# Performance work log

Hardware: AMD Instinct MI355X
Metric: run time of the kernel (lower is better)

## Reference

```python
import jax, jax.numpy as jnp
import numpy as np
from math import sqrt


def setup_inputs() -> dict:
    key = jax.random.key(0)
    k1, k2, k3, k4, k5 = jax.random.split(key, 5)
    B, L, H, D = 16, 4096, 16, 64
    S, M = 4096, 256
    queries = jax.random.normal(k1, (B, L, H, D), dtype=jnp.float32)
    keys = jax.random.normal(k2, (B, S, H, D), dtype=jnp.float32)
    values = jax.random.normal(k3, (B, S, H, D), dtype=jnp.float32)
    # nn.Linear(L_k=S, M): weight [M, S], bias [M]
    squeeze_w = jax.random.normal(k4, (M, S), dtype=jnp.float32) / sqrt(S)
    squeeze_b = jax.random.normal(k5, (M,), dtype=jnp.float32) * 0.01
    return {"queries": queries, "keys": keys, "values": values,
            "squeeze_w": squeeze_w, "squeeze_b": squeeze_b}


def reference(queries, keys, values, squeeze_w, squeeze_b):
    # queries: [B,L,H,D]; keys/values: [B,S,H,D]; squeeze_w: [M,S]; squeeze_b: [M]
    B, L, H, D = queries.shape
    scale = 1.0 / sqrt(D)
    bias = squeeze_b[None, :, None, None]  # broadcast over [B,M,H,D]
    # Linear over the sequence axis S -> M (Linformer compression)
    keys_sq = jnp.einsum('bshd,ms->bmhd', keys, squeeze_w) + bias      # [B,M,H,D]
    values_sq = jnp.einsum('bshd,ms->bmhd', values, squeeze_w) + bias  # [B,M,H,D]
    # Scaled dot-product attention against compressed K/V
    attn = jnp.einsum('blhd,bmhd->bhlm', queries, keys_sq) * scale     # [B,H,L,M]
    attn = jax.nn.softmax(attn, axis=-1)  # dropout is identity in eval / p=0
    context = jnp.einsum('bhlm,bmhd->blhd', attn, values_sq)           # [B,L,H,D]
    return context
```

## Files before the change

kernel.cpp:

```cpp
#include <hip/hip_runtime.h>

#define NB 16
#define NL 4096
#define NH 16
#define ND 64
#define NS 4096
#define NM 256

typedef __fp16 f16;
typedef __attribute__((ext_vector_type(8)))  __fp16 f16x8;
typedef __attribute__((ext_vector_type(4)))  __fp16 f16x4;
typedef __attribute__((ext_vector_type(2)))  __fp16 f16x2;
typedef __attribute__((ext_vector_type(4)))  float  f32x4;
typedef __attribute__((ext_vector_type(16))) float  f32x16;

__device__ __forceinline__ void gload_lds16(const void* g, void* l) {
  __builtin_amdgcn_global_load_lds(
      (const __attribute__((address_space(1))) void*)g,
      (__attribute__((address_space(3))) void*)l, 16, 0, 0);
}

__device__ __forceinline__ int pk2(float a, float b) {
  f16x2 t = __builtin_amdgcn_cvt_pkrtz(a, b);
  union { f16x2 h; int i; } u; u.h = t; return u.i;
}

__global__ __launch_bounds__(256) void k_wcvt(const float* __restrict__ W,
                                              f16* __restrict__ Wk) {
  const int o  = blockIdx.x * 256 + threadIdx.x;
  const int m  = o & 255;
  const int kb = o >> 8;
  const float* src = W + (long)m * NS + kb * 8;
  f32x4 v0 = *(const f32x4*)(src);
  f32x4 v1 = *(const f32x4*)(src + 4);
  union { f16x8 v; f16x2 h2[4]; } pk;
  pk.h2[0] = __builtin_amdgcn_cvt_pkrtz(v0[0], v0[1]);
  pk.h2[1] = __builtin_amdgcn_cvt_pkrtz(v0[2], v0[3]);
  pk.h2[2] = __builtin_amdgcn_cvt_pkrtz(v1[0], v1[1]);
  pk.h2[3] = __builtin_amdgcn_cvt_pkrtz(v1[2], v1[3]);
  *(f16x8*)(Wk + (long)o * 8) = pk.v;
}

__global__ __launch_bounds__(512, 4) void k_squeeze(
    const f16* __restrict__ Wk, const float* __restrict__ keys,
    const float* __restrict__ values, const float* __restrict__ bias,
    f16* __restrict__ Ksq, f16* __restrict__ Vsq) {
  const int h = blockIdx.x & 15;
  const int b = (blockIdx.x >> 4) & 15;
  const int t = blockIdx.x >> 8;
  const float* __restrict__ X = t ? values : keys;

  __shared__ __align__(16) f16 XT0[64 * 72];
  __shared__ __align__(16) f16 XT1[64 * 72];

  const int tid  = threadIdx.x;
  const int lane = tid & 63;
  const int w    = tid >> 6;
  const int l31  = lane & 31;
  const int g    = lane >> 5;

  const int sp = tid & 31;
  const int ng = tid >> 5;
  const float* Xb = X + ((long)b * NS) * (NH * ND) + h * ND;

  f32x16 acc[2];
#pragma unroll
  for (int di = 0; di < 2; ++di)
#pragma unroll
    for (int r = 0; r < 16; ++r) acc[di][r] = 0.f;

  f32x4 xrA[2], xrB[2];
#pragma unroll
  for (int r = 0; r < 2; ++r)
    xrA[r] = *(const f32x4*)(Xb + (long)(2 * sp + r) * (NH * ND) + ng * 4);
#pragma unroll
  for (int r = 0; r < 2; ++r)
    xrB[r] = *(const f32x4*)(Xb + (long)(64 + 2 * sp + r) * (NH * ND) + ng * 4);

  const f16* Wlane = Wk + ((long)g * 256 + w * 32 + l31) * 8;

  for (int kt2 = 0; kt2 < 32; ++kt2) {
    {
      const int kt = 2 * kt2;
      f16x8 af[4];
#pragma unroll
      for (int ks = 0; ks < 4; ++ks)
        af[ks] = *(const f16x8*)(Wlane + ((long)(kt * 8 + ks * 2) * 256) * 8);
      int p0 = pk2(xrA[0][0], xrA[1][0]);
      int p1 = pk2(xrA[0][1], xrA[1][1]);
      int p2 = pk2(xrA[0][2], xrA[1][2]);
      int p3 = pk2(xrA[0][3], xrA[1][3]);
      if (kt2 < 31) {
#pragma unroll
        for (int r = 0; r < 2; ++r)
          xrA[r] = *(const f32x4*)(Xb + (long)((kt + 2) * 64 + 2 * sp + r) * (NH * ND) + ng * 4);
      }
      *(int*)((char*)XT0 + (ng * 4 + 0) * 144 + sp * 4) = p0;
      *(int*)((char*)XT0 + (ng * 4 + 1) * 144 + sp * 4) = p1;
      *(int*)((char*)XT0 + (ng * 4 + 2) * 144 + sp * 4) = p2;
      *(int*)((char*)XT0 + (ng * 4 + 3) * 144 + sp * 4) = p3;
      __syncthreads();
#pragma unroll
      for (int ks = 0; ks < 4; ++ks) {
        f16x8 bf0 = *(const f16x8*)((const char*)XT0 + l31 * 144 + ks * 32 + g * 16);
        f16x8 bf1 = *(const f16x8*)((const char*)XT0 + (32 + l31) * 144 + ks * 32 + g * 16);
        acc[0] = __builtin_amdgcn_mfma_f32_32x32x16_f16(af[ks], bf0, acc[0], 0, 0, 0);
        acc[1] = __builtin_amdgcn_mfma_f32_32x32x16_f16(af[ks], bf1, acc[1], 0, 0, 0);
      }
    }
    {
      const int kt = 2 * kt2 + 1;
      f16x8 af[4];
#pragma unroll
      for (int ks = 0; ks < 4; ++ks)
        af[ks] = *(const f16x8*)(Wlane + ((long)(kt * 8 + ks * 2) * 256) * 8);
      int p0 = pk2(xrB[0][0], xrB[1][0]);
      int p1 = pk2(xrB[0][1], xrB[1][1]);
      int p2 = pk2(xrB[0][2], xrB[1][2]);
      int p3 = pk2(xrB[0][3], xrB[1][3]);
      if (kt2 < 31) {
#pragma unroll
        for (int r = 0; r < 2; ++r)
          xrB[r] = *(const f32x4*)(Xb + (long)((kt + 2) * 64 + 2 * sp + r) * (NH * ND) + ng * 4);
      }
      *(int*)((char*)XT1 + (ng * 4 + 0) * 144 + sp * 4) = p0;
      *(int*)((char*)XT1 + (ng * 4 + 1) * 144 + sp * 4) = p1;
      *(int*)((char*)XT1 + (ng * 4 + 2) * 144 + sp * 4) = p2;
      *(int*)((char*)XT1 + (ng * 4 + 3) * 144 + sp * 4) = p3;
      __syncthreads();
#pragma unroll
      for (int ks = 0; ks < 4; ++ks) {
        f16x8 bf0 = *(const f16x8*)((const char*)XT1 + l31 * 144 + ks * 32 + g * 16);
        f16x8 bf1 = *(const f16x8*)((const char*)XT1 + (32 + l31) * 144 + ks * 32 + g * 16);
        acc[0] = __builtin_amdgcn_mfma_f32_32x32x16_f16(af[ks], bf0, acc[0], 0, 0, 0);
        acc[1] = __builtin_amdgcn_mfma_f32_32x32x16_f16(af[ks], bf1, acc[1], 0, 0, 0);
      }
    }
  }

  const long bh = b * 16 + h;
  if (t == 0) {
    f16* K = Ksq + bh * (NM * ND);
#pragma unroll
    for (int di = 0; di < 2; ++di)
#pragma unroll
      for (int r = 0; r < 16; ++r) {
        const int m = w * 32 + (r & 3) + 8 * (r >> 2) + 4 * g;
        const int d = di * 32 + l31;
        K[((d >> 3) * 256 + m) * 8 + (d & 7)] = (f16)(acc[di][r] + bias[m]);
      }
  } else {
    f16* V = Vsq + bh * (ND * NM);
#pragma unroll
    for (int di = 0; di < 2; ++di)
#pragma unroll
      for (int qq = 0; qq < 4; ++qq) {
        const int m0 = w * 32 + 8 * qq + 4 * g;
        const int d  = di * 32 + l31;
        f16x2 p0 = __builtin_amdgcn_cvt_pkrtz(acc[di][qq * 4 + 0] + bias[m0 + 0],
                                              acc[di][qq * 4 + 1] + bias[m0 + 1]);
        f16x2 p1 = __builtin_amdgcn_cvt_pkrtz(acc[di][qq * 4 + 2] + bias[m0 + 2],
                                              acc[di][qq * 4 + 3] + bias[m0 + 3]);
        f16x4 pv; pv[0] = p0[0]; pv[1] = p0[1]; pv[2] = p1[0]; pv[3] = p1[1];
        *(f16x4*)(V + ((m0 >> 3) * 64 + d) * 8 + 4 * g) = pv;
      }
  }
}

__global__ __launch_bounds__(256, 2) void k_attn(const float* __restrict__ Q,
                                                 const f16* __restrict__ Ksq,
                                                 const f16* __restrict__ Vsq,
                                                 float* __restrict__ Out) {
  const int xcd   = blockIdx.x & 7;
  const int local = blockIdx.x >> 3;
  const int bh    = xcd * 32 + (local >> 1);
  const int chunk = local & 1;
  const int b = bh >> 4, h = bh & 15;

  __shared__ __align__(16) f16 Klds[8 * 256 * 8];
  __shared__ __align__(16) f16 Vlds[32 * 64 * 8];

  const int tid = threadIdx.x, lane = tid & 63, w = tid >> 6;
  const int q = lane & 31, hi = lane >> 5;

  const float* Qlane = Q   + (((long)b * NL + q) * NH + h) * ND;
  float*       Olane = Out + (((long)b * NL + q) * NH + h) * ND;
  const float  c = 0.125f * 1.44269504088896f;

  f32x4 qv[8];
  {
    const float* qp = Qlane + (long)(chunk * 2048 + w * 32) * (NH * ND) + hi * 8;
#pragma unroll
    for (int kt = 0; kt < 4; ++kt) {
      qv[2 * kt]     = *(const f32x4*)(qp + kt * 16);
      qv[2 * kt + 1] = *(const f32x4*)(qp + kt * 16 + 4);
    }
  }

  {
    const f16* Kg = Ksq + (long)bh * 16384;
    const f16* Vg = Vsq + (long)bh * 16384;
#pragma unroll
    for (int i = 0; i < 8; ++i)
      gload_lds16(Kg + w * 4096 + i * 512 + lane * 8, (char*)Klds + w * 8192 + i * 1024);
#pragma unroll
    for (int i = 0; i < 8; ++i)
      gload_lds16(Vg + w * 4096 + i * 512 + lane * 8, (char*)Vlds + w * 8192 + i * 1024);
  }
  __syncthreads();

  for (int it = 0; it < 16; ++it) {
    const int row0 = chunk * 2048 + it * 128 + w * 32;

    union { f16x8 v; f16x2 h2[4]; } qb[4];
#pragma unroll
    for (int kt = 0; kt < 4; ++kt) {
      qb[kt].h2[0] = __builtin_amdgcn_cvt_pkrtz(qv[2 * kt][0], qv[2 * kt][1]);
      qb[kt].h2[1] = __builtin_amdgcn_cvt_pkrtz(qv[2 * kt][2], qv[2 * kt][3]);
      qb[kt].h2[2] = __builtin_amdgcn_cvt_pkrtz(qv[2 * kt + 1][0], qv[2 * kt + 1][1]);
      qb[kt].h2[3] = __builtin_amdgcn_cvt_pkrtz(qv[2 * kt + 1][2], qv[2 * kt + 1][3]);
    }

    if (it + 1 < 16) {
      const float* qp = Qlane + (long)(row0 + 128) * (NH * ND) + hi * 8;
#pragma unroll
      for (int kt = 0; kt < 4; ++kt) {
        qv[2 * kt]     = *(const f32x4*)(qp + kt * 16);
        qv[2 * kt + 1] = *(const f32x4*)(qp + kt * 16 + 4);
      }
    }

    f32x16 sa[8];
#pragma unroll
    for (int mf = 0; mf < 8; ++mf)
#pragma unroll
      for (int r = 0; r < 16; ++r) sa[mf][r] = 0.f;

#pragma unroll
    for (int kt = 0; kt < 4; ++kt) {
#pragma unroll
      for (int mf = 0; mf < 8; ++mf) {
        f16x8 ka = *(const f16x8*)((const char*)Klds +
                                   ((2 * kt + hi) * 256 + mf * 32 + q) * 16);
        sa[mf] = __builtin_amdgcn_mfma_f32_32x32x16_f16(ka, qb[kt].v, sa[mf], 0, 0, 0);
      }
    }

    f32x16 mm = sa[0];
#pragma unroll
    for (int mf = 1; mf < 8; ++mf)
#pragma unroll
      for (int r = 0; r < 16; ++r) mm[r] = fmaxf(mm[r], sa[mf][r]);
    float m8_0 = fmaxf(mm[0], mm[8]),  m8_1 = fmaxf(mm[1], mm[9]);
    float m8_2 = fmaxf(mm[2], mm[10]), m8_3 = fmaxf(mm[3], mm[11]);
    float m8_4 = fmaxf(mm[4], mm[12]), m8_5 = fmaxf(mm[5], mm[13]);
    float m8_6 = fmaxf(mm[6], mm[14]), m8_7 = fmaxf(mm[7], mm[15]);
    float mx = fmaxf(fmaxf(fmaxf(m8_0, m8_1), fmaxf(m8_2, m8_3)),
                     fmaxf(fmaxf(m8_4, m8_5), fmaxf(m8_6, m8_7)));
    mx = fmaxf(mx, __shfl_xor(mx, 32));

#pragma unroll
    for (int mf = 0; mf < 8; ++mf)
#pragma unroll
      for (int r = 0; r < 16; ++r)
        sa[mf][r] = __builtin_amdgcn_exp2f((sa[mf][r] - mx) * c);

    f32x16 t0 = sa[0] + sa[1];
    f32x16 t1 = sa[2] + sa[3];
    f32x16 t2 = sa[4] + sa[5];
    f32x16 t3 = sa[6] + sa[7];
    t0 = (t0 + t1) + (t2 + t3);
    float s8_0 = t0[0] + t0[8],  s8_1 = t0[1] + t0[9];
    float s8_2 = t0[2] + t0[10], s8_3 = t0[3] + t0[11];
    float s8_4 = t0[4] + t0[12], s8_5 = t0[5] + t0[13];
    float s8_6 = t0[6] + t0[14], s8_7 = t0[7] + t0[15];
    float sum = ((s8_0 + s8_1) + (s8_2 + s8_3)) + ((s8_4 + s8_5) + (s8_6 + s8_7));
    sum += __shfl_xor(sum, 32);
    const float inv = 1.0f / sum;

    f32x16 o[2];
#pragma unroll
    for (int df = 0; df < 2; ++df)
#pragma unroll
      for (int r = 0; r < 16; ++r) o[df][r] = 0.f;

#pragma unroll
    for (int t = 0; t < 16; ++t) {
      const int fp = t >> 1, s = t & 1;
      int a0 = pk2(sa[fp][8 * s + 0] * inv, sa[fp][8 * s + 1] * inv);
      int a1 = pk2(sa[fp][8 * s + 2] * inv, sa[fp][8 * s + 3] * inv);
      int b0 = pk2(sa[fp][8 * s + 4] * inv, sa[fp][8 * s + 5] * inv);
      int b1 = pk2(sa[fp][8 * s + 6] * inv, sa[fp][8 * s + 7] * inv);
      asm volatile("v_permlane32_swap_b32 %0, %1" : "+v"(a0), "+v"(b0));
      asm volatile("v_permlane32_swap_b32 %0, %1" : "+v"(a1), "+v"(b1));
      union { int w4[4]; f16x8 v; } pb;
      pb.w4[0] = a0; pb.w4[1] = a1; pb.w4[2] = b0; pb.w4[3] = b1;
#pragma unroll
      for (int df = 0; df < 2; ++df) {
        f16x8 va = *(const f16x8*)((const char*)Vlds +
                                   ((2 * t + hi) * 64 + df * 32 + q) * 16);
        o[df] = __builtin_amdgcn_mfma_f32_32x32x16_f16(va, pb.v, o[df], 0, 0, 0);
      }
    }

    float* op = Olane + (long)row0 * (NH * ND);
#pragma unroll
    for (int df = 0; df < 2; ++df)
#pragma unroll
      for (int rq = 0; rq < 4; ++rq) {
        f32x4 st;
        st[0] = o[df][rq * 4 + 0]; st[1] = o[df][rq * 4 + 1];
        st[2] = o[df][rq * 4 + 2]; st[3] = o[df][rq * 4 + 3];
        *(f32x4*)(op + df * 32 + rq * 8 + hi * 4) = st;
      }
  }
}

extern "C" void kernel_launch(void* const* d_in, const int* in_sizes, int n_in,
                              void* d_out, int out_size, void* d_ws, size_t ws_size,
                              hipStream_t stream) {
  const float* Qp   = (const float*)d_in[0];
  const float* Kp   = (const float*)d_in[1];
  const float* Vp   = (const float*)d_in[2];
  const float* Wp   = (const float*)d_in[3];
  const float* bp   = (const float*)d_in[4];
  float*       Outp = (float*)d_out;

  char* ws = (char*)d_ws;
  f16* Wk  = (f16*)ws;
  f16* Ksq = (f16*)(ws + (2l << 20));
  f16* Vsq = (f16*)(ws + (2l << 20) + (8l << 20));

  hipLaunchKernelGGL(k_wcvt, dim3(512), dim3(256), 0, stream, Wp, Wk);
  hipLaunchKernelGGL(k_squeeze, dim3(512), dim3(512), 0, stream, Wk, Kp, Vp, bp, Ksq, Vsq);
  hipLaunchKernelGGL(k_attn, dim3(512), dim3(256), 0, stream, Qp, Ksq, Vsq, Outp);
}
```

Before: 315.3 us.

## Split squeeze GEMM over sequence halves with separate reduction kernel

The squeeze kernel now splits the S=4096 reduction into two halves, launching 1024 blocks instead of 512, and writes fp32 partial results to a workspace buffer. A new reduce kernel sums the two partials, adds the bias, and writes the fp16 K/V layouts that the attention kernel expects. The aim is more parallelism and better CU occupancy in the bandwidth-heavy squeeze stage. The cost is an extra kernel launch plus writing and reading 32 MB of fp32 partials.

```diff
diff --git a/kernel.cpp b/kernel.cpp
--- a/kernel.cpp
+++ b/kernel.cpp
@@ -41,13 +41,13 @@
   *(f16x8*)(Wk + (long)o * 8) = pk.v;
 }
 
-__global__ __launch_bounds__(512, 4) void k_squeeze(
+__global__ __launch_bounds__(512, 4) void k_squeeze_p(
     const f16* __restrict__ Wk, const float* __restrict__ keys,
-    const float* __restrict__ values, const float* __restrict__ bias,
-    f16* __restrict__ Ksq, f16* __restrict__ Vsq) {
-  const int h = blockIdx.x & 15;
-  const int b = (blockIdx.x >> 4) & 15;
-  const int t = blockIdx.x >> 8;
+    const float* __restrict__ values, float* __restrict__ P) {
+  const int h  = blockIdx.x & 15;
+  const int b  = (blockIdx.x >> 4) & 15;
+  const int sq = (blockIdx.x >> 8) & 1;
+  const int t  = blockIdx.x >> 9;
   const float* __restrict__ X = t ? values : keys;
 
   __shared__ __align__(16) f16 XT0[64 * 72];
@@ -61,7 +61,7 @@
 
   const int sp = tid & 31;
   const int ng = tid >> 5;
-  const float* Xb = X + ((long)b * NS) * (NH * ND) + h * ND;
+  const float* Xb = X + ((long)b * NS + sq * 2048) * (NH * ND) + h * ND;
 
   f32x16 acc[2];
 #pragma unroll
@@ -77,9 +77,9 @@
   for (int r = 0; r < 2; ++r)
     xrB[r] = *(const f32x4*)(Xb + (long)(64 + 2 * sp + r) * (NH * ND) + ng * 4);
 
-  const f16* Wlane = Wk + ((long)g * 256 + w * 32 + l31) * 8;
-
-  for (int kt2 = 0; kt2 < 32; ++kt2) {
+  const f16* Wlane = Wk + ((long)sq * 256 * 256 + (long)g * 256 + w * 32 + l31) * 8;
+
+  for (int kt2 = 0; kt2 < 16; ++kt2) {
     {
       const int kt = 2 * kt2;
       f16x8 af[4];
@@ -90,7 +90,7 @@
       int p1 = pk2(xrA[0][1], xrA[1][1]);
       int p2 = pk2(xrA[0][2], xrA[1][2]);
       int p3 = pk2(xrA[0][3], xrA[1][3]);
-      if (kt2 < 31) {
+      if (kt2 < 15) {
 #pragma unroll
         for (int r = 0; r < 2; ++r)
           xrA[r] = *(const f32x4*)(Xb + (long)((kt + 2) * 64 + 2 * sp + r) * (NH * ND) + ng * 4);
@@ -118,7 +118,7 @@
       int p1 = pk2(xrB[0][1], xrB[1][1]);
       int p2 = pk2(xrB[0][2], xrB[1][2]);
       int p3 = pk2(xrB[0][3], xrB[1][3]);
-      if (kt2 < 31) {
+      if (kt2 < 15) {
 #pragma unroll
         for (int r = 0; r < 2; ++r)
           xrB[r] = *(const f32x4*)(Xb + (long)((kt + 2) * 64 + 2 * sp + r) * (NH * ND) + ng * 4);
@@ -139,31 +139,52 @@
   }
 
   const long bh = b * 16 + h;
-  if (t == 0) {
-    f16* K = Ksq + bh * (NM * ND);
-#pragma unroll
-    for (int di = 0; di < 2; ++di)
-#pragma unroll
-      for (int r = 0; r < 16; ++r) {
-        const int m = w * 32 + (r & 3) + 8 * (r >> 2) + 4 * g;
-        const int d = di * 32 + l31;
-        K[((d >> 3) * 256 + m) * 8 + (d & 7)] = (f16)(acc[di][r] + bias[m]);
-      }
-  } else {
-    f16* V = Vsq + bh * (ND * NM);
-#pragma unroll
-    for (int di = 0; di < 2; ++di)
-#pragma unroll
-      for (int qq = 0; qq < 4; ++qq) {
-        const int m0 = w * 32 + 8 * qq + 4 * g;
-        const int d  = di * 32 + l31;
-        f16x2 p0 = __builtin_amdgcn_cvt_pkrtz(acc[di][qq * 4 + 0] + bias[m0 + 0],
-                                              acc[di][qq * 4 + 1] + bias[m0 + 1]);
-        f16x2 p1 = __builtin_amdgcn_cvt_pkrtz(acc[di][qq * 4 + 2] + bias[m0 + 2],
-                                              acc[di][qq * 4 + 3] + bias[m0 + 3]);
-        f16x4 pv; pv[0] = p0[0]; pv[1] = p0[1]; pv[2] = p1[0]; pv[3] = p1[1];
-        *(f16x4*)(V + ((m0 >> 3) * 64 + d) * 8 + 4 * g) = pv;
-      }
+  float* Pb = P + (((long)t * 256 + bh) * 2 + sq) * (NM * ND);
+#pragma unroll
+  for (int di = 0; di < 2; ++di) {
+    const int d = di * 32 + l31;
+#pragma unroll
+    for (int rq = 0; rq < 4; ++rq) {
+      const int m0 = w * 32 + rq * 8 + g * 4;
+      f32x4 st;
+      st[0] = acc[di][rq * 4 + 0]; st[1] = acc[di][rq * 4 + 1];
+      st[2] = acc[di][rq * 4 + 2]; st[3] = acc[di][rq * 4 + 3];
+      *(f32x4*)(Pb + d * 256 + m0) = st;
+    }
+  }
+}
+
+__global__ __launch_bounds__(256) void k_reduce(const float* __restrict__ P,
+                                                const float* __restrict__ bias,
+                                                f16* __restrict__ Ksq,
+                                                f16* __restrict__ Vsq) {
+  const int bh = blockIdx.x & 255;
+  const int t  = blockIdx.x >> 8;
+  const float* P0 = P + (((long)t * 256 + bh) * 2 + 0) * (NM * ND);
+  const float* P1 = P + (((long)t * 256 + bh) * 2 + 1) * (NM * ND);
+  const int tid = threadIdx.x;
+
+#pragma unroll
+  for (int i = 0; i < 16; ++i) {
+    const int v = i * 256 + tid;
+    const int d = v >> 6;
+    const int m = (v & 63) * 4;
+    f32x4 a = *(const f32x4*)(P0 + d * 256 + m);
+    f32x4 bv = *(const f32x4*)(P1 + d * 256 + m);
+    f32x4 bb = *(const f32x4*)(bias + m);
+    f32x4 s = a + bv + bb;
+    if (t == 0) {
+      f16* K = Ksq + (long)bh * (NM * ND);
+#pragma unroll
+      for (int j = 0; j < 4; ++j)
+        K[((d >> 3) * 256 + m + j) * 8 + (d & 7)] = (f16)s[j];
+    } else {
+      f16* V = Vsq + (long)bh * (ND * NM);
+      f16x2 q0 = __builtin_amdgcn_cvt_pkrtz(s[0], s[1]);
+      f16x2 q1 = __builtin_amdgcn_cvt_pkrtz(s[2], s[3]);
+      f16x4 pv; pv[0] = q0[0]; pv[1] = q0[1]; pv[2] = q1[0]; pv[3] = q1[1];
+      *(f16x4*)(V + ((m >> 3) * 64 + d) * 8 + (m & 7)) = pv;
+    }
   }
 }
 
@@ -327,11 +348,13 @@
   float*       Outp = (float*)d_out;
 
   char* ws = (char*)d_ws;
-  f16* Wk  = (f16*)ws;
-  f16* Ksq = (f16*)(ws + (2l << 20));
-  f16* Vsq = (f16*)(ws + (2l << 20) + (8l << 20));
+  f16*   Wk  = (f16*)ws;
+  f16*   Ksq = (f16*)(ws + (2l << 20));
+  f16*   Vsq = (f16*)(ws + (10l << 20));
+  float* P   = (float*)(ws + (18l << 20));
 
   hipLaunchKernelGGL(k_wcvt, dim3(512), dim3(256), 0, stream, Wp, Wk);
-  hipLaunchKernelGGL(k_squeeze, dim3(512), dim3(512), 0, stream, Wk, Kp, Vp, bp, Ksq, Vsq);
+  hipLaunchKernelGGL(k_squeeze_p, dim3(1024), dim3(512), 0, stream, Wk, Kp, Vp, P);
+  hipLaunchKernelGGL(k_reduce, dim3(512), dim3(256), 0, stream, P, bp, Ksq, Vsq);
   hipLaunchKernelGGL(k_attn, dim3(512), dim3(256), 0, stream, Qp, Ksq, Vsq, Outp);
 }
```

Result: slower. 349.5 us (+10.8%).

## Prefetch squeeze weights one k-tile ahead and barrier without draining global loads

Applied to the files above, without the earlier changes.

In the squeeze GEMM, the fp16 weight fragments for the next k-tile are now loaded into a second register set before the current tile's MFMAs run. The per-tile __syncthreads is replaced by a barrier that waits only on LDS operations (lgkmcnt), so in-flight global loads of X and W keep running across the barrier. The aim is to hide global-load latency behind MFMA work. The cost is extra VGPRs for the second fragment set, which can lower occupancy. Correctness also relies on vmcnt waits being inserted where the registers are later used.

```diff
diff --git a/kernel.cpp b/kernel.cpp
--- a/kernel.cpp
+++ b/kernel.cpp
@@ -23,6 +23,13 @@
 __device__ __forceinline__ int pk2(float a, float b) {
   f16x2 t = __builtin_amdgcn_cvt_pkrtz(a, b);
   union { f16x2 h; int i; } u; u.h = t; return u.i;
+}
+
+__device__ __forceinline__ void sync_nodrain() {
+  asm volatile("s_waitcnt lgkmcnt(0)" ::: "memory");
+  __builtin_amdgcn_sched_barrier(0);
+  __builtin_amdgcn_s_barrier();
+  __builtin_amdgcn_sched_barrier(0);
 }
 
 __global__ __launch_bounds__(256) void k_wcvt(const float* __restrict__ W,
@@ -78,14 +85,17 @@
     xrB[r] = *(const f32x4*)(Xb + (long)(64 + 2 * sp + r) * (NH * ND) + ng * 4);
 
   const f16* Wlane = Wk + ((long)g * 256 + w * 32 + l31) * 8;
+  f16x8 afA[4], afB[4];
+#pragma unroll
+  for (int ks = 0; ks < 4; ++ks)
+    afA[ks] = *(const f16x8*)(Wlane + ((long)(ks * 2) * 256) * 8);
 
   for (int kt2 = 0; kt2 < 32; ++kt2) {
     {
       const int kt = 2 * kt2;
-      f16x8 af[4];
 #pragma unroll
       for (int ks = 0; ks < 4; ++ks)
-        af[ks] = *(const f16x8*)(Wlane + ((long)(kt * 8 + ks * 2) * 256) * 8);
+        afB[ks] = *(const f16x8*)(Wlane + ((long)((kt + 1) * 8 + ks * 2) * 256) * 8);
       int p0 = pk2(xrA[0][0], xrA[1][0]);
       int p1 = pk2(xrA[0][1], xrA[1][1]);
       int p2 = pk2(xrA[0][2], xrA[1][2]);
@@ -99,21 +109,22 @@
       *(int*)((char*)XT0 + (ng * 4 + 1) * 144 + sp * 4) = p1;
       *(int*)((char*)XT0 + (ng * 4 + 2) * 144 + sp * 4) = p2;
       *(int*)((char*)XT0 + (ng * 4 + 3) * 144 + sp * 4) = p3;
-      __syncthreads();
+      sync_nodrain();
 #pragma unroll
       for (int ks = 0; ks < 4; ++ks) {
         f16x8 bf0 = *(const f16x8*)((const char*)XT0 + l31 * 144 + ks * 32 + g * 16);
         f16x8 bf1 = *(const f16x8*)((const char*)XT0 + (32 + l31) * 144 + ks * 32 + g * 16);
-        acc[0] = __builtin_amdgcn_mfma_f32_32x32x16_f16(af[ks], bf0, acc[0], 0, 0, 0);
-        acc[1] = __builtin_amdgcn_mfma_f32_32x32x16_f16(af[ks], bf1, acc[1], 0, 0, 0);
+        acc[0] = __builtin_amdgcn_mfma_f32_32x32x16_f16(afA[ks], bf0, acc[0], 0, 0, 0);
+        acc[1] = __builtin_amdgcn_mfma_f32_32x32x16_f16(afA[ks], bf1, acc[1], 0, 0, 0);
       }
     }
     {
       const int kt = 2 * kt2 + 1;
-      f16x8 af[4];
-#pragma unroll
-      for (int ks = 0; ks < 4; ++ks)
-        af[ks] = *(const f16x8*)(Wlane + ((long)(kt * 8 + ks * 2) * 256) * 8);
+      if (kt2 < 31) {
+#pragma unroll
+        for (int ks = 0; ks < 4; ++ks)
+          afA[ks] = *(const f16x8*)(Wlane + ((long)((kt + 1) * 8 + ks * 2) * 256) * 8);
+      }
       int p0 = pk2(xrB[0][0], xrB[1][0]);
       int p1 = pk2(xrB[0][1], xrB[1][1]);
       int p2 = pk2(xrB[0][2], xrB[1][2]);
@@ -127,13 +138,13 @@
       *(int*)((char*)XT1 + (ng * 4 + 1) * 144 + sp * 4) = p1;
       *(int*)((char*)XT1 + (ng * 4 + 2) * 144 + sp * 4) = p2;
       *(int*)((char*)XT1 + (ng * 4 + 3) * 144 + sp * 4) = p3;
-      __syncthreads();
+      sync_nodrain();
 #pragma unroll
       for (int ks = 0; ks < 4; ++ks) {
         f16x8 bf0 = *(const f16x8*)((const char*)XT1 + l31 * 144 + ks * 32 + g * 16);
         f16x8 bf1 = *(const f16x8*)((const char*)XT1 + (32 + l31) * 144 + ks * 32 + g * 16);
-        acc[0] = __builtin_amdgcn_mfma_f32_32x32x16_f16(af[ks], bf0, acc[0], 0, 0, 0);
-        acc[1] = __builtin_amdgcn_mfma_f32_32x32x16_f16(af[ks], bf1, acc[1], 0, 0, 0);
+        acc[0] = __builtin_amdgcn_mfma_f32_32x32x16_f16(afB[ks], bf0, acc[0], 0, 0, 0);
+        acc[1] = __builtin_amdgcn_mfma_f32_32x32x16_f16(afB[ks], bf1, acc[1], 0, 0, 0);
       }
     }
   }
@@ -329,7 +340,7 @@
   char* ws = (char*)d_ws;
   f16* Wk  = (f16*)ws;
   f16* Ksq = (f16*)(ws + (2l << 20));
-  f16* Vsq = (f16*)(ws + (2l << 20) + (8l << 20));
+  f16* Vsq = (f16*)(ws + (10l << 20));
 
   hipLaunchKernelGGL(k_wcvt, dim3(512), dim3(256), 0, stream, Wp, Wk);
   hipLaunchKernelGGL(k_squeeze, dim3(512), dim3(512), 0, stream, Wk, Kp, Vp, bp, Ksq, Vsq);
```

Result: no change. 317.5 us (+0.7%).
